# Kernel tuning notes

Hardware: AMD Instinct MI355X
Metric: run time of the kernel (lower is better)

The kernel has to match this reference:

```python
import jax, jax.numpy as jnp
import numpy as np

N_SUB = 262144      # total subgraphs (rows of h_subgraph)
NUM_GRAPHS = 8192   # graphs in batch
D = 128             # channel width
L = 3               # number of fc / fc_sum layers
NUM_TASKS = 10


def segment_mean(x, idx, num_segments):
    # scatter_mean: sum per segment, divide by count (count>=1 guard like torch_scatter)
    sums = jax.ops.segment_sum(x, idx, num_segments=num_segments)
    cnt = jax.ops.segment_sum(jnp.ones((x.shape[0],), dtype=x.dtype), idx, num_segments=num_segments)
    return sums / jnp.maximum(cnt, 1.0)[:, None]


def setup_inputs() -> dict:
    key = jax.random.key(0)
    ks = jax.random.split(key, 10)
    s = 1.0 / np.sqrt(D)
    h_subgraph = jax.random.normal(ks[0], (N_SUB, D), dtype=jnp.float32)
    subgraph_idx = jnp.sort(jax.random.randint(ks[1], (N_SUB,), 0, NUM_GRAPHS, dtype=jnp.int32))
    W_fc = jax.random.normal(ks[2], (L, D, D), dtype=jnp.float32) * s
    b_fc = jax.random.normal(ks[3], (L, D), dtype=jnp.float32) * s
    W_sum = jax.random.normal(ks[4], (L, D, D), dtype=jnp.float32) * s
    b_sum = jax.random.normal(ks[5], (L, D), dtype=jnp.float32) * s
    W_f1 = jax.random.normal(ks[6], (D, 2 * D), dtype=jnp.float32) * s
    b_f1 = jax.random.normal(ks[7], (2 * D,), dtype=jnp.float32) * s
    W_f2 = jax.random.normal(ks[8], (2 * D, NUM_TASKS), dtype=jnp.float32) / np.sqrt(2 * D)
    b_f2 = jax.random.normal(ks[9], (NUM_TASKS,), dtype=jnp.float32) / np.sqrt(2 * D)
    return {"h_subgraph": h_subgraph, "subgraph_idx": subgraph_idx,
            "W_fc": W_fc, "b_fc": b_fc, "W_sum": W_sum, "b_sum": b_sum,
            "W_f1": W_f1, "b_f1": b_f1, "W_f2": W_f2, "b_f2": b_f2}


def reference(h_subgraph, subgraph_idx, W_fc, b_fc, W_sum, b_sum, W_f1, b_f1, W_f2, b_f2):
    h = h_subgraph
    # non-invariant branch: per-layer Linear + scatter_mean + Linear + gather + ELU
    for i in range(L):
        x1 = h @ W_fc[i] + b_fc[i]                                  # [N, D]
        g = segment_mean(h, subgraph_idx, NUM_GRAPHS)               # [G, D]
        x2 = g @ W_sum[i] + b_sum[i]                                # [G, D]
        h = jax.nn.elu(x1 + x2[subgraph_idx])                       # gather + combine
    h_graph = segment_mean(h, subgraph_idx, NUM_GRAPHS)             # [G, D]
    # final MLP head
    out = jax.nn.relu(h_graph @ W_f1 + b_f1) @ W_f2 + b_f2          # [G, num_tasks]
    return out
```

## Files before the change

### kernel.cpp

```cpp
#include <hip/hip_runtime.h>

#define NSUB 262144
#define NG   8192
#define DIM  128
#define NT   10

typedef __attribute__((ext_vector_type(4))) float f32x4;
typedef __attribute__((ext_vector_type(8))) short short8;
typedef unsigned short ushort_t;
typedef unsigned int uint_t;

__device__ __forceinline__ float bf2f(ushort_t u){
    union { uint_t i; float f; } v; v.i = ((uint_t)u) << 16; return v.f;
}
__device__ __forceinline__ ushort_t f2bf(float f){
    union { __bf16 b; ushort_t u; } v; v.b = (__bf16)f; return v.u;
}


__global__ __launch_bounds__(256) void zero_kernel(float* __restrict__ g,
                                                   float* __restrict__ cnt)
{
    const long t = (long)blockIdx.x * 256 + threadIdx.x;
    if (t < 524288) ((f32x4*)g)[t] = (f32x4){0.f, 0.f, 0.f, 0.f};
    else            ((f32x4*)cnt)[t - 524288] = (f32x4){0.f, 0.f, 0.f, 0.f};
}

__global__ __launch_bounds__(256) void wprep_kernel(const float* __restrict__ Wfc,
                                                    ushort_t* __restrict__ Wt)
{
    int t = blockIdx.x * 256 + threadIdx.x;
    int i   = t >> 11;
    int rem = t & 2047;
    int ks  = rem >> 9;
    int f   = (rem >> 6) & 7;
    int l   = rem & 63;
    int c   = f * 16 + (l & 15);
    int kb  = ks * 32 + (l >> 4) * 8;
    short8 v;
    #pragma unroll
    for (int j = 0; j < 8; j++)
        v[j] = (short)f2bf(Wfc[i * 16384 + (kb + j) * 128 + c]);
    *(short8*)(Wt + (long)t * 8) = v;
}

__global__ __launch_bounds__(256) void conv0_kernel(const float* __restrict__ h0,
                                                    const int* __restrict__ idx,
                                                    ushort_t* __restrict__ hfrag,
                                                    float* __restrict__ gsum,
                                                    float* __restrict__ cnt)
{
    __shared__ int sidx[128];
    __shared__ __align__(16) char fb[128 * 272];
    const int tid = threadIdx.x;
    const long base = (long)blockIdx.x * 128;
    if (tid < 128) sidx[tid] = idx[base + tid];
    __syncthreads();

    const int cg = tid & 31, ch = tid >> 5;
    const int rloc0 = ch * 16;

    f32x4 v[16];
    #pragma unroll
    for (int j = 0; j < 16; j++)
        v[j] = *(const f32x4*)(h0 + (base + rloc0 + j) * 128 + cg * 4);
    #pragma unroll
    for (int j = 0; j < 16; j++){
        uint2 pk;
        pk.x = (uint_t)f2bf(v[j][0]) | ((uint_t)f2bf(v[j][1]) << 16);
        pk.y = (uint_t)f2bf(v[j][2]) | ((uint_t)f2bf(v[j][3]) << 16);
        *(uint2*)(fb + (rloc0 + j) * 272 + cg * 8) = pk;
    }

    f32x4 acc = {0.f, 0.f, 0.f, 0.f};
    int cur = sidx[rloc0], n = 0;
    #pragma unroll
    for (int j = 0; j < 16; j++){
        const int g = sidx[rloc0 + j];
        if (g != cur){
            float* gp = gsum + (long)cur * 128 + cg * 4;
            atomicAdd(gp + 0, acc[0]); atomicAdd(gp + 1, acc[1]);
            atomicAdd(gp + 2, acc[2]); atomicAdd(gp + 3, acc[3]);
            if (cg == 0) atomicAdd(cnt + cur, (float)n);
            acc = {0.f, 0.f, 0.f, 0.f}; n = 0; cur = g;
        }
        acc += v[j]; n++;
    }
    float* gp = gsum + (long)cur * 128 + cg * 4;
    atomicAdd(gp + 0, acc[0]); atomicAdd(gp + 1, acc[1]);
    atomicAdd(gp + 2, acc[2]); atomicAdd(gp + 3, acc[3]);
    if (cg == 0) atomicAdd(cnt + cur, (float)n);
    __syncthreads();

    const int r15 = tid & 15, grp = (tid >> 4) & 3, ks = tid >> 6;
    f32x4* dst = (f32x4*)hfrag + (long)blockIdx.x * 2048 + tid;
    const char* srcrow = fb + ks * 64 + grp * 16;
    #pragma unroll
    for (int rg = 0; rg < 8; rg++){
        f32x4 val = *(const f32x4*)(srcrow + (rg * 16 + r15) * 272);
        dst[rg * 256] = val;
    }
}

__global__ __launch_bounds__(256) void x2_kernel(float* g,
                                                 const float* __restrict__ cnt,
                                                 const float* __restrict__ Wsum,
                                                 const float* __restrict__ bsum,
                                                 const float* __restrict__ bfc,
                                                 float* __restrict__ x2)
{
    __shared__ float gm[16][128];
    __shared__ float invc[16];
    const int tid = threadIdx.x;
    const int r0 = blockIdx.x * 16;
    if (tid < 16) invc[tid] = 1.f / fmaxf(cnt[r0 + tid], 1.f);
    __syncthreads();
    #pragma unroll
    for (int p = 0; p < 8; p++){
        int e = tid + p * 256;
        int row = e >> 7, col = e & 127;
        float val = g[(long)(r0 + row) * 128 + col];
        gm[row][col] = val * invc[row];
        g[(long)(r0 + row) * 128 + col] = 0.f;
    }
    __syncthreads();
    const int c = tid & 127, rh = tid >> 7;
    float acc[8];
    #pragma unroll
    for (int i = 0; i < 8; i++) acc[i] = bsum[c] + bfc[c];
    for (int k = 0; k < 128; k++){
        float w = Wsum[k * 128 + c];
        #pragma unroll
        for (int i = 0; i < 8; i++) acc[i] += gm[rh * 8 + i][k] * w;
    }
    #pragma unroll
    for (int i = 0; i < 8; i++) x2[(long)(r0 + rh * 8 + i) * 128 + c] = acc[i];
}

__global__ __launch_bounds__(256) void layer_kernel(ushort_t* hbuf,
                                                    const ushort_t* __restrict__ Wt,
                                                    const float* __restrict__ x2,
                                                    const int* __restrict__ idx,
                                                    float* __restrict__ gnext)
{
    __shared__ __align__(16) ushort_t seg[128 * 132];
    __shared__ int sidx[128];
    const int tid = threadIdx.x;
    const long base = (long)blockIdx.x * 128;
    if (tid < 128) sidx[tid] = idx[base + tid];
    __syncthreads();

    const int wv = tid >> 6, ln = tid & 63;
    const int ln15 = ln & 15, grp = ln >> 4;
    const long Rbase = (long)blockIdx.x * 8 + wv * 2;

    f32x4 acc[2][8];
    #pragma unroll
    for (int q = 0; q < 2; q++)
        #pragma unroll
        for (int f = 0; f < 8; f++) acc[q][f] = {0.f, 0.f, 0.f, 0.f};

    #pragma unroll
    for (int ks = 0; ks < 4; ks++){
        short8 a[8];
        #pragma unroll
        for (int f = 0; f < 8; f++)
            a[f] = *(const short8*)(Wt + ((long)(ks * 8 + f) * 64 + ln) * 8);
        short8 b[2];
        #pragma unroll
        for (int q = 0; q < 2; q++)
            b[q] = *(const short8*)(hbuf + (((Rbase + q) * 4 + ks) * 64 + ln) * 8);
        #pragma unroll
        for (int q = 0; q < 2; q++)
            #pragma unroll
            for (int f = 0; f < 8; f++)
                acc[q][f] = __builtin_amdgcn_mfma_f32_16x16x32_bf16(a[f], b[q], acc[q][f], 0, 0, 0);
    }

    #pragma unroll
    for (int q = 0; q < 2; q++){
        const int lr = wv * 32 + q * 16 + ln15;
        const int g = sidx[lr];
        const float* x2r = x2 + (long)g * 128;
        #pragma unroll
        for (int f = 0; f < 8; f++){
            const int cb = f * 16 + grp * 4;
            f32x4 xv = *(const f32x4*)(x2r + cb);
            ushort_t h4[4];
            #pragma unroll
            for (int i = 0; i < 4; i++){
                float v = acc[q][f][i] + xv[i];
                v = v > 0.f ? v : (__expf(v) - 1.f);
                h4[i] = f2bf(v);
            }
            uint2 pk;
            pk.x = (uint_t)h4[0] | ((uint_t)h4[1] << 16);
            pk.y = (uint_t)h4[2] | ((uint_t)h4[3] << 16);
            const long c16 = ((Rbase + q) * 4 + (f >> 1)) * 64
                           + (2 * (f & 1) + (grp >> 1)) * 16 + ln15;
            *(uint2*)((char*)hbuf + c16 * 16 + (grp & 1) * 8) = pk;
            *(uint2*)((char*)seg + lr * 264 + cb * 2) = pk;
        }
    }
    __syncthreads();

    const int c = tid & 63, ch2 = tid >> 6;
    const int rr0 = ch2 * 32;
    float a0 = 0.f, a1 = 0.f;
    int cur = sidx[rr0];
    for (int j = 0; j < 32; j++){
        const int rr = rr0 + j;
        const int g = sidx[rr];
        if (g != cur){
            atomicAdd(gnext + (long)cur * 128 + 2 * c,     a0);
            atomicAdd(gnext + (long)cur * 128 + 2 * c + 1, a1);
            a0 = a1 = 0.f; cur = g;
        }
        uint_t u = *(const uint_t*)((const char*)seg + rr * 264 + c * 4);
        a0 += bf2f((ushort_t)(u & 0xffff));
        a1 += bf2f((ushort_t)(u >> 16));
    }
    atomicAdd(gnext + (long)cur * 128 + 2 * c,     a0);
    atomicAdd(gnext + (long)cur * 128 + 2 * c + 1, a1);
}

__global__ __launch_bounds__(256) void head_kernel(const float* __restrict__ g,
                                                   const float* __restrict__ cnt,
                                                   const float* __restrict__ Wf1,
                                                   const float* __restrict__ bf1,
                                                   const float* __restrict__ Wf2,
                                                   const float* __restrict__ bf2,
                                                   float* __restrict__ out)
{
    __shared__ float hm[8][128];
    __shared__ float t1[8][256];
    __shared__ float invc[8];
    const int tid = threadIdx.x;
    const int r0 = blockIdx.x * 8;
    if (tid < 8) invc[tid] = 1.f / fmaxf(cnt[r0 + tid], 1.f);
    __syncthreads();
    #pragma unroll
    for (int p = 0; p < 4; p++){
        int e = tid + p * 256;
        int row = e >> 7, col = e & 127;
        hm[row][col] = g[(long)(r0 + row) * 128 + col] * invc[row];
    }
    __syncthreads();
    {
        const int c = tid;
        float acc[8];
        #pragma unroll
        for (int r = 0; r < 8; r++) acc[r] = bf1[c];
        for (int k = 0; k < 128; k++){
            float w = Wf1[k * 256 + c];
            #pragma unroll
            for (int r = 0; r < 8; r++) acc[r] += hm[r][k] * w;
        }
        #pragma unroll
        for (int r = 0; r < 8; r++) t1[r][c] = fmaxf(acc[r], 0.f);
    }
    __syncthreads();
    if (tid < 80){
        const int r = tid / 10, c = tid % 10;
        float acc = bf2[c];
        for (int k = 0; k < 256; k++) acc += t1[r][k] * Wf2[k * 10 + c];
        out[(long)(r0 + r) * 10 + c] = acc;
    }
}

extern "C" void kernel_launch(void* const* d_in, const int* in_sizes, int n_in,
                              void* d_out, int out_size, void* d_ws, size_t ws_size,
                              hipStream_t stream)
{
    const float* h0   = (const float*)d_in[0];
    const int*   idx  = (const int*)d_in[1];
    const float* Wfc  = (const float*)d_in[2];
    const float* bfc  = (const float*)d_in[3];
    const float* Wsum = (const float*)d_in[4];
    const float* bsum = (const float*)d_in[5];
    const float* Wf1  = (const float*)d_in[6];
    const float* bf1  = (const float*)d_in[7];
    const float* Wf2  = (const float*)d_in[8];
    const float* bf2  = (const float*)d_in[9];
    float* out = (float*)d_out;

    char* ws = (char*)d_ws;
    ushort_t* hbuf = (ushort_t*)ws;
    float* g0  = (float*)(ws + 67108864);
    float* g1  = (float*)(ws + 71303168);
    float* x2  = (float*)(ws + 75497472);
    float* cnt = (float*)(ws + 79691776);
    ushort_t* Wt = (ushort_t*)(ws + 79724544);
    if (ws_size < 79822848ull) return;

    zero_kernel<<<2056, 256, 0, stream>>>(g0, cnt);
    wprep_kernel<<<24, 256, 0, stream>>>(Wfc, Wt);

    conv0_kernel<<<NSUB / 128, 256, 0, stream>>>(h0, idx, hbuf, g0, cnt);
    x2_kernel<<<NG / 16, 256, 0, stream>>>(g0, cnt, Wsum, bsum, bfc, x2);
    layer_kernel<<<NSUB / 128, 256, 0, stream>>>(hbuf, Wt, x2, idx, g1);

    x2_kernel<<<NG / 16, 256, 0, stream>>>(g1, cnt, Wsum + 16384, bsum + 128, bfc + 128, x2);
    layer_kernel<<<NSUB / 128, 256, 0, stream>>>(hbuf, Wt + 16384, x2, idx, g0);

    x2_kernel<<<NG / 16, 256, 0, stream>>>(g0, cnt, Wsum + 32768, bsum + 256, bfc + 256, x2);
    layer_kernel<<<NSUB / 128, 256, 0, stream>>>(hbuf, Wt + 32768, x2, idx, g1);

    head_kernel<<<NG / 8, 256, 0, stream>>>(g1, cnt, Wf1, bf1, Wf2, bf2, out);
}
```

Measured before the change: 255.3 us.

## Merge prep kernels, swizzle block order, prefetch operands in layer kernel

Merges the zero and weight-prep kernels into one launch to save a launch. Remaps block indices in conv0 and layer kernels with a stride-8 swizzle, likely to spread work across XCDs or L2 partitions. In layer_kernel, all hbuf fragments are loaded up front, weight loads are split into two halves interleaved with MFMAs, x2 gathers are hoisted ahead of the epilogue, and launch_bounds asks for 4 blocks per CU. More registers are held live, and the swizzle may hurt locality for the segment atomics.

```diff
diff --git a/kernel.cpp b/kernel.cpp
--- a/kernel.cpp
+++ b/kernel.cpp
@@ -18,30 +18,32 @@
 }
 
 
-__global__ __launch_bounds__(256) void zero_kernel(float* __restrict__ g,
+__global__ __launch_bounds__(256) void prep_kernel(const float* __restrict__ Wfc,
+                                                   ushort_t* __restrict__ Wt,
+                                                   float* __restrict__ g,
                                                    float* __restrict__ cnt)
 {
-    const long t = (long)blockIdx.x * 256 + threadIdx.x;
-    if (t < 524288) ((f32x4*)g)[t] = (f32x4){0.f, 0.f, 0.f, 0.f};
-    else            ((f32x4*)cnt)[t - 524288] = (f32x4){0.f, 0.f, 0.f, 0.f};
-}
-
-__global__ __launch_bounds__(256) void wprep_kernel(const float* __restrict__ Wfc,
-                                                    ushort_t* __restrict__ Wt)
-{
-    int t = blockIdx.x * 256 + threadIdx.x;
-    int i   = t >> 11;
-    int rem = t & 2047;
-    int ks  = rem >> 9;
-    int f   = (rem >> 6) & 7;
-    int l   = rem & 63;
-    int c   = f * 16 + (l & 15);
-    int kb  = ks * 32 + (l >> 4) * 8;
-    short8 v;
-    #pragma unroll
-    for (int j = 0; j < 8; j++)
-        v[j] = (short)f2bf(Wfc[i * 16384 + (kb + j) * 128 + c]);
-    *(short8*)(Wt + (long)t * 8) = v;
+    const int b = blockIdx.x;
+    if (b < 2056){
+        const long t = (long)b * 256 + threadIdx.x;
+        const f32x4 z = {0.f, 0.f, 0.f, 0.f};
+        if (t < 524288) ((f32x4*)g)[t] = z;
+        else            ((f32x4*)cnt)[t - 524288] = z;
+    } else {
+        int t = (b - 2056) * 256 + threadIdx.x;
+        int i   = t >> 11;
+        int rem = t & 2047;
+        int ks  = rem >> 9;
+        int f   = (rem >> 6) & 7;
+        int l   = rem & 63;
+        int c   = f * 16 + (l & 15);
+        int kb  = ks * 32 + (l >> 4) * 8;
+        short8 v;
+        #pragma unroll
+        for (int j = 0; j < 8; j++)
+            v[j] = (short)f2bf(Wfc[i * 16384 + (kb + j) * 128 + c]);
+        *(short8*)(Wt + (long)t * 8) = v;
+    }
 }
 
 __global__ __launch_bounds__(256) void conv0_kernel(const float* __restrict__ h0,
@@ -53,7 +55,8 @@
     __shared__ int sidx[128];
     __shared__ __align__(16) char fb[128 * 272];
     const int tid = threadIdx.x;
-    const long base = (long)blockIdx.x * 128;
+    const int bid = ((blockIdx.x & 7) << 8) | (blockIdx.x >> 3);
+    const long base = (long)bid * 128;
     if (tid < 128) sidx[tid] = idx[base + tid];
     __syncthreads();
 
@@ -93,7 +96,7 @@
     __syncthreads();
 
     const int r15 = tid & 15, grp = (tid >> 4) & 3, ks = tid >> 6;
-    f32x4* dst = (f32x4*)hfrag + (long)blockIdx.x * 2048 + tid;
+    f32x4* dst = (f32x4*)hfrag + (long)bid * 2048 + tid;
     const char* srcrow = fb + ks * 64 + grp * 16;
     #pragma unroll
     for (int rg = 0; rg < 8; rg++){
@@ -137,7 +140,7 @@
     for (int i = 0; i < 8; i++) x2[(long)(r0 + rh * 8 + i) * 128 + c] = acc[i];
 }
 
-__global__ __launch_bounds__(256) void layer_kernel(ushort_t* hbuf,
+__global__ __launch_bounds__(256, 4) void layer_kernel(ushort_t* hbuf,
                                                     const ushort_t* __restrict__ Wt,
                                                     const float* __restrict__ x2,
                                                     const int* __restrict__ idx,
@@ -146,13 +149,21 @@
     __shared__ __align__(16) ushort_t seg[128 * 132];
     __shared__ int sidx[128];
     const int tid = threadIdx.x;
-    const long base = (long)blockIdx.x * 128;
+    const int bid = ((blockIdx.x & 7) << 8) | (blockIdx.x >> 3);
+    const long base = (long)bid * 128;
     if (tid < 128) sidx[tid] = idx[base + tid];
     __syncthreads();
 
     const int wv = tid >> 6, ln = tid & 63;
     const int ln15 = ln & 15, grp = ln >> 4;
-    const long Rbase = (long)blockIdx.x * 8 + wv * 2;
+    const long Rbase = (long)bid * 8 + wv * 2;
+
+    short8 b8[8];
+    #pragma unroll
+    for (int ks = 0; ks < 4; ks++)
+        #pragma unroll
+        for (int q = 0; q < 2; q++)
+            b8[ks * 2 + q] = *(const short8*)(hbuf + (((Rbase + q) * 4 + ks) * 64 + ln) * 8);
 
     f32x4 acc[2][8];
     #pragma unroll
@@ -162,19 +173,23 @@
 
     #pragma unroll
     for (int ks = 0; ks < 4; ks++){
-        short8 a[8];
-        #pragma unroll
-        for (int f = 0; f < 8; f++)
-            a[f] = *(const short8*)(Wt + ((long)(ks * 8 + f) * 64 + ln) * 8);
-        short8 b[2];
-        #pragma unroll
-        for (int q = 0; q < 2; q++)
-            b[q] = *(const short8*)(hbuf + (((Rbase + q) * 4 + ks) * 64 + ln) * 8);
-        #pragma unroll
-        for (int q = 0; q < 2; q++)
+        short8 a0[4], a1[4];
+        #pragma unroll
+        for (int f = 0; f < 4; f++)
+            a0[f] = *(const short8*)(Wt + ((long)(ks * 8 + f) * 64 + ln) * 8);
+        #pragma unroll
+        for (int f = 0; f < 4; f++)
             #pragma unroll
-            for (int f = 0; f < 8; f++)
-                acc[q][f] = __builtin_amdgcn_mfma_f32_16x16x32_bf16(a[f], b[q], acc[q][f], 0, 0, 0);
+            for (int q = 0; q < 2; q++)
+                acc[q][f] = __builtin_amdgcn_mfma_f32_16x16x32_bf16(a0[f], b8[ks * 2 + q], acc[q][f], 0, 0, 0);
+        #pragma unroll
+        for (int f = 0; f < 4; f++)
+            a1[f] = *(const short8*)(Wt + ((long)(ks * 8 + 4 + f) * 64 + ln) * 8);
+        #pragma unroll
+        for (int f = 0; f < 4; f++)
+            #pragma unroll
+            for (int q = 0; q < 2; q++)
+                acc[q][4 + f] = __builtin_amdgcn_mfma_f32_16x16x32_bf16(a1[f], b8[ks * 2 + q], acc[q][4 + f], 0, 0, 0);
     }
 
     #pragma unroll
@@ -182,14 +197,17 @@
         const int lr = wv * 32 + q * 16 + ln15;
         const int g = sidx[lr];
         const float* x2r = x2 + (long)g * 128;
+        f32x4 xv[8];
+        #pragma unroll
+        for (int f = 0; f < 8; f++)
+            xv[f] = *(const f32x4*)(x2r + f * 16 + grp * 4);
         #pragma unroll
         for (int f = 0; f < 8; f++){
             const int cb = f * 16 + grp * 4;
-            f32x4 xv = *(const f32x4*)(x2r + cb);
             ushort_t h4[4];
             #pragma unroll
             for (int i = 0; i < 4; i++){
-                float v = acc[q][f][i] + xv[i];
+                float v = acc[q][f][i] + xv[f][i];
                 v = v > 0.f ? v : (__expf(v) - 1.f);
                 h4[i] = f2bf(v);
             }
@@ -293,8 +311,7 @@
     ushort_t* Wt = (ushort_t*)(ws + 79724544);
     if (ws_size < 79822848ull) return;
 
-    zero_kernel<<<2056, 256, 0, stream>>>(g0, cnt);
-    wprep_kernel<<<24, 256, 0, stream>>>(Wfc, Wt);
+    prep_kernel<<<2080, 256, 0, stream>>>(Wfc, Wt, g0, cnt);
 
     conv0_kernel<<<NSUB / 128, 256, 0, stream>>>(h0, idx, hbuf, g0, cnt);
     x2_kernel<<<NG / 16, 256, 0, stream>>>(g0, cnt, Wsum, bsum, bfc, x2);
```

Result: faster. 240.6 us (-5.8%).
